# Kernel tuning notes

Measured on AMD Instinct MI355X. Metric: run time of the kernel, lower is better.

The kernel has to match this reference:

```python
import jax, jax.numpy as jnp
import numpy as np
from jax import lax

ALPHA = 0.1
HIDDEN_DIM = 512


def setup_inputs() -> dict:
    key = jax.random.key(0)
    ks = jax.random.split(key, 8)
    B, T, I, H, O, R = 64, 1024, 128, 512, 512, 2
    x = jax.random.normal(ks[0], (B, T, I), dtype=jnp.float32)
    h0 = jnp.zeros((B, H), dtype=jnp.float32)
    Wxh = jax.random.normal(ks[1], (H, I), dtype=jnp.float32) / np.sqrt(I)
    bxh = jax.random.normal(ks[2], (H,), dtype=jnp.float32) * 0.01
    U = jax.random.normal(ks[3], (H, R), dtype=jnp.float32) / np.sqrt(H)
    V = jax.random.normal(ks[4], (H, R), dtype=jnp.float32) / np.sqrt(H)
    Why = jax.random.normal(ks[5], (O, H), dtype=jnp.float32) / np.sqrt(H)
    bhy = jax.random.normal(ks[6], (O,), dtype=jnp.float32) * 0.01
    return {"x": x, "h0": h0, "Wxh": Wxh, "bxh": bxh, "U": U, "V": V,
            "Why": Why, "bhy": bhy}


def reference(x, h0, Wxh, bxh, U, V, Why, bhy):
    # x: (B,T,I); precompute the input projection for all timesteps at once
    xproj = jnp.einsum('bti,hi->bth', x, Wxh) + bxh  # (B,T,H)

    def step(h, xp_t):
        # low-rank recurrent map: h @ V @ U.T / hidden_dim
        pre = xp_t + (h @ V) @ U.T / HIDDEN_DIM  # (B,H)
        h_new = (1.0 - ALPHA) * h + ALPHA * jnp.tanh(pre)
        return h_new, h_new

    _, hs = lax.scan(step, h0, jnp.swapaxes(xproj, 0, 1))  # hs: (T,B,H)
    h_all = jnp.swapaxes(hs, 0, 1)  # (B,T,H)
    y = jnp.einsum('bth,oh->bto', h_all, Why) + bhy  # (B,T,O)
    return y, h_all
```

## Files before the change

### kernel.cpp

```cpp
#include <hip/hip_runtime.h>
#include <hip/hip_bf16.h>
#include <cstdint>

#define B_ 64
#define T_ 1024
#define I_ 128
#define H_ 512
#define O_ 512

#define CHUNK_L 64
#define NCHUNK (T_ / CHUNK_L)
#define WARM_ 96

typedef short bf16x8 __attribute__((ext_vector_type(8)));
typedef float f32x4 __attribute__((ext_vector_type(4)));

typedef const __attribute__((address_space(1))) void* gptr_t;
typedef __attribute__((address_space(3))) void* lptr_t;

__device__ __forceinline__ unsigned short f2bf(float f) {
    unsigned int u = __float_as_uint(f);
    u += 0x7fffu + ((u >> 16) & 1u);
    return (unsigned short)(u >> 16);
}
__device__ __forceinline__ float bf2f(unsigned short b) {
    return __uint_as_float(((unsigned int)b) << 16);
}
__device__ __forceinline__ float fast_tanh(float x) {
    float e = __builtin_amdgcn_exp2f(x * 2.8853900817779268f);
    return 1.0f - 2.0f * __builtin_amdgcn_rcpf(e + 1.0f);
}

template <int CTRL>
__device__ __forceinline__ float dpp_add(float v) {
    int t = __builtin_amdgcn_update_dpp(0, __float_as_int(v), CTRL, 0xf, 0xf, true);
    return v + __int_as_float(t);
}
__device__ __forceinline__ float wave_sum64(float v) {
    v = dpp_add<0x111>(v);
    v = dpp_add<0x112>(v);
    v = dpp_add<0x114>(v);
    v = dpp_add<0x118>(v);
    v = dpp_add<0x142>(v);
    v = dpp_add<0x143>(v);
    return __uint_as_float(__builtin_amdgcn_readlane(__float_as_uint(v), 63));
}

#define NX_ (B_ * T_ * I_)
#define NW_ (H_ * I_)
#define NY_ (O_ * H_)

__global__ __launch_bounds__(256)
void cast_all(const float* __restrict__ x, const float* __restrict__ Wxh,
              const float* __restrict__ Why, unsigned short* __restrict__ xb,
              unsigned short* __restrict__ wb, unsigned short* __restrict__ yb) {
    int i4 = (blockIdx.x * 256 + threadIdx.x) * 4;
    const float* s;
    unsigned short* d;
    int off;
    if (i4 < NX_)             { s = x;   d = xb; off = i4; }
    else if (i4 < NX_ + NW_)  { s = Wxh; d = wb; off = i4 - NX_; }
    else                      { s = Why; d = yb; off = i4 - NX_ - NW_; }
    float4 v = *(const float4*)(s + off);
    ushort4 o;
    o.x = f2bf(v.x); o.y = f2bf(v.y); o.z = f2bf(v.z); o.w = f2bf(v.w);
    *(ushort4*)(d + off) = o;
}

template <bool STORE_BF16>
__global__ __launch_bounds__(256)
void gemm_bt(const unsigned short* __restrict__ A,
             const unsigned short* __restrict__ Bm,
             const float* __restrict__ bias,
             void* __restrict__ Cout,
             int M, int N, int K) {
    __shared__ unsigned short As[128 * 32];
    __shared__ unsigned short Bs[128 * 32];

    const int tid  = threadIdx.x;
    const int lane = tid & 63;
    const int w    = tid >> 6;
    const int wm   = (w >> 1) * 64;
    const int wn   = (w & 1) * 64;
    const int nblk = N >> 7;
    const int bm   = (int)(blockIdx.x / nblk) << 7;
    const int bn   = (int)(blockIdx.x % nblk) << 7;

    f32x4 acc[4][4] = {};

    const int srow = tid >> 2;
    const int scol = (tid & 3) << 3;
    const unsigned short* gA0 = A  + (size_t)(bm + srow) * K + scol;
    const unsigned short* gA1 = A  + (size_t)(bm + 64 + srow) * K + scol;
    const unsigned short* gB0 = Bm + (size_t)(bn + srow) * K + scol;
    const unsigned short* gB1 = Bm + (size_t)(bn + 64 + srow) * K + scol;

    unsigned short* ldsA0 = As + w * 512;
    unsigned short* ldsA1 = As + 2048 + w * 512;
    unsigned short* ldsB0 = Bs + w * 512;
    unsigned short* ldsB1 = Bs + 2048 + w * 512;

    const int frow = lane & 15;
    const int fk   = (lane >> 4) << 3;

    for (int kt = 0; kt < K; kt += 32) {
        __syncthreads();
        __builtin_amdgcn_global_load_lds((gptr_t)(gA0 + kt), (lptr_t)ldsA0, 16, 0, 0);
        __builtin_amdgcn_global_load_lds((gptr_t)(gA1 + kt), (lptr_t)ldsA1, 16, 0, 0);
        __builtin_amdgcn_global_load_lds((gptr_t)(gB0 + kt), (lptr_t)ldsB0, 16, 0, 0);
        __builtin_amdgcn_global_load_lds((gptr_t)(gB1 + kt), (lptr_t)ldsB1, 16, 0, 0);
        __syncthreads();

        bf16x8 af[4], bf[4];
#pragma unroll
        for (int mt = 0; mt < 4; ++mt)
            af[mt] = *(const bf16x8*)(As + (wm + mt * 16 + frow) * 32 + fk);
#pragma unroll
        for (int nt = 0; nt < 4; ++nt)
            bf[nt] = *(const bf16x8*)(Bs + (wn + nt * 16 + frow) * 32 + fk);
#pragma unroll
        for (int mt = 0; mt < 4; ++mt)
#pragma unroll
            for (int nt = 0; nt < 4; ++nt)
                acc[mt][nt] = __builtin_amdgcn_mfma_f32_16x16x32_bf16(
                    af[mt], bf[nt], acc[mt][nt], 0, 0, 0);
    }

    const int c_col = lane & 15;
    const int c_row = (lane >> 4) << 2;
#pragma unroll
    for (int nt = 0; nt < 4; ++nt) {
        const int gn = bn + wn + nt * 16 + c_col;
        const float bv = bias[gn];
#pragma unroll
        for (int mt = 0; mt < 4; ++mt) {
            const int gm0 = bm + wm + mt * 16 + c_row;
#pragma unroll
            for (int r = 0; r < 4; ++r) {
                float v = acc[mt][nt][r] + bv;
                size_t idx = (size_t)(gm0 + r) * N + gn;
                if (STORE_BF16) ((unsigned short*)Cout)[idx] = f2bf(v);
                else            ((float*)Cout)[idx] = v;
            }
        }
    }
}

__global__ __launch_bounds__(64)
void scan_kernel(const unsigned short* __restrict__ xproj,
                 const float* __restrict__ h0,
                 const float* __restrict__ U,
                 const float* __restrict__ V,
                 float* __restrict__ hall_f32,
                 unsigned short* __restrict__ hall_bf) {
    const int blk = blockIdx.x;
    const int b = blk / NCHUNK;
    const int c = blk % NCHUNK;
    const int t_start = c * CHUNK_L;
    const int t0 = (t_start - WARM_ > 0) ? (t_start - WARM_) : 0;
    const int nwarm = t_start - t0;
    const int NT = nwarm + CHUNK_L;

    const int lane = threadIdx.x;
    const int hbase = lane * 8;

    const float inv_h = 1.0f / (float)H_;
    float h[8], V0[8], V1[8], U0[8], U1[8];
#pragma unroll
    for (int j = 0; j < 8; ++j) {
        V0[j] = V[(hbase + j) * 2 + 0] * inv_h;
        V1[j] = V[(hbase + j) * 2 + 1] * inv_h;
        U0[j] = U[(hbase + j) * 2 + 0];
        U1[j] = U[(hbase + j) * 2 + 1];
    }
    if (t0 == 0) {
#pragma unroll
        for (int j = 0; j < 8; ++j) h[j] = h0[b * H_ + hbase + j];
    } else {
#pragma unroll
        for (int j = 0; j < 8; ++j) h[j] = 0.f;
    }

    const unsigned short* xp = xproj + ((size_t)b * T_ + t0) * H_ + hbase;
    float* ho = hall_f32 + (size_t)b * T_ * H_ + hbase;
    unsigned short* hb = hall_bf + (size_t)b * T_ * H_ + hbase;

    float s0 = 0.f, s1 = 0.f;
    if (t0 == 0) {
        float a0 = 0.f, a1 = 0.f;
#pragma unroll
        for (int j = 0; j < 8; ++j) { a0 += h[j] * V0[j]; a1 += h[j] * V1[j]; }
        s0 = wave_sum64(a0);
        s1 = wave_sum64(a1);
    }

    uint4 xq0, xq1, xq2, xq3;
#define LOADX(DST, IDX)                                                        \
    if ((IDX) < NT) DST = *(const uint4*)(xp + (size_t)(IDX) * H_);
    xq0 = *(const uint4*)xp;
    LOADX(xq1, 1)
    LOADX(xq2, 2)
    LOADX(xq3, 3)

#define SCAN_SLOT(REG, IDX, DO_STORE)                                          \
    {                                                                          \
        uint4 xc = REG;                                                        \
        LOADX(REG, (IDX) + 4)                                                  \
        float xp8[8];                                                          \
        {                                                                      \
            unsigned int uu[4] = {xc.x, xc.y, xc.z, xc.w};                     \
            _Pragma("unroll")                                                  \
            for (int q = 0; q < 4; ++q) {                                      \
                xp8[2 * q + 0] = bf2f((unsigned short)(uu[q] & 0xffffu));      \
                xp8[2 * q + 1] = bf2f((unsigned short)(uu[q] >> 16));          \
            }                                                                  \
        }                                                                      \
        float g[8];                                                            \
        _Pragma("unroll")                                                      \
        for (int j = 0; j < 8; ++j)                                            \
            g[j] = fast_tanh(xp8[j] + s0 * U0[j] + s1 * U1[j]);                \
        _Pragma("unroll")                                                      \
        for (int j = 0; j < 8; ++j)                                            \
            h[j] = 0.9f * h[j] + 0.1f * g[j];                                  \
        float p0a = 0.f, p0b = 0.f, p1a = 0.f, p1b = 0.f;                      \
        _Pragma("unroll")                                                      \
        for (int j = 0; j < 4; ++j) {                                          \
            p0a += g[j] * V0[j];       p0b += g[j + 4] * V0[j + 4];            \
            p1a += g[j] * V1[j];       p1b += g[j + 4] * V1[j + 4];            \
        }                                                                      \
        float r0 = wave_sum64(p0a + p0b);                                      \
        float r1 = wave_sum64(p1a + p1b);                                      \
        s0 = 0.9f * s0 + 0.1f * r0;                                            \
        s1 = 0.9f * s1 + 0.1f * r1;                                            \
        if (DO_STORE) {                                                        \
            const size_t tt = (size_t)(t0 + (IDX));                            \
            float4 v0 = make_float4(h[0], h[1], h[2], h[3]);                   \
            float4 v1 = make_float4(h[4], h[5], h[6], h[7]);                   \
            *(float4*)(ho + tt * H_ + 0) = v0;                                 \
            *(float4*)(ho + tt * H_ + 4) = v1;                                 \
            uint4 pb;                                                          \
            pb.x = ((unsigned int)f2bf(h[1]) << 16) | f2bf(h[0]);              \
            pb.y = ((unsigned int)f2bf(h[3]) << 16) | f2bf(h[2]);              \
            pb.z = ((unsigned int)f2bf(h[5]) << 16) | f2bf(h[4]);              \
            pb.w = ((unsigned int)f2bf(h[7]) << 16) | f2bf(h[6]);              \
            *(uint4*)(hb + tt * H_) = pb;                                      \
        }                                                                      \
    }

    int I = 0;
    for (; I < nwarm; I += 4) {
        SCAN_SLOT(xq0, I + 0, false)
        SCAN_SLOT(xq1, I + 1, false)
        SCAN_SLOT(xq2, I + 2, false)
        SCAN_SLOT(xq3, I + 3, false)
    }
    for (; I < NT; I += 4) {
        SCAN_SLOT(xq0, I + 0, true)
        SCAN_SLOT(xq1, I + 1, true)
        SCAN_SLOT(xq2, I + 2, true)
        SCAN_SLOT(xq3, I + 3, true)
    }
#undef SCAN_SLOT
#undef LOADX
}

extern "C" void kernel_launch(void* const* d_in, const int* in_sizes, int n_in,
                              void* d_out, int out_size, void* d_ws, size_t ws_size,
                              hipStream_t stream) {
    const float* x   = (const float*)d_in[0];
    const float* h0  = (const float*)d_in[1];
    const float* Wxh = (const float*)d_in[2];
    const float* bxh = (const float*)d_in[3];
    const float* U   = (const float*)d_in[4];
    const float* V   = (const float*)d_in[5];
    const float* Why = (const float*)d_in[6];
    const float* bhy = (const float*)d_in[7];

    float* y    = (float*)d_out;
    float* hall = y + (size_t)B_ * T_ * O_;

    unsigned short* x_bf    = (unsigned short*)d_ws;
    unsigned short* Wxh_bf  = x_bf + (size_t)B_ * T_ * I_;
    unsigned short* Why_bf  = Wxh_bf + (size_t)H_ * I_;
    unsigned short* xp_bf   = Why_bf + (size_t)O_ * H_;
    unsigned short* hall_bf = xp_bf + (size_t)B_ * T_ * H_;

    cast_all<<<(NX_ + NW_ + NY_) / 1024, 256, 0, stream>>>(
        x, Wxh, Why, x_bf, Wxh_bf, Why_bf);

    gemm_bt<true><<<dim3((B_ * T_ / 128) * (H_ / 128)), 256, 0, stream>>>(
        x_bf, Wxh_bf, bxh, xp_bf, B_ * T_, H_, I_);

    scan_kernel<<<B_ * NCHUNK, 64, 0, stream>>>(xp_bf, h0, U, V, hall, hall_bf);

    gemm_bt<false><<<dim3((B_ * T_ / 128) * (O_ / 128)), 256, 0, stream>>>(
        hall_bf, Why_bf, bhy, y, B_ * T_, O_, H_);
}
```

Measured before the change: 466.7 us.

## Stage GEMM epilogue through padded LDS for coalesced vector stores; branchless scan prefetch

The GEMM epilogue now writes accumulators plus bias into a padded shared-memory tile one 16-row slab at a time, then reads them back so each thread issues 16-byte global stores (float4 or 8 bf16s) instead of scattered scalar stores. This targets the uncoalesced output writes of the input projection and output GEMMs. In exchange it adds LDS usage and two barriers per slab, which may reduce occupancy. Separately, the scan's prefetch loads are made branchless by clamping the index to the last valid timestep, which removes divergent conditionals at the cost of a few redundant loads.

```diff
diff --git a/kernel.cpp b/kernel.cpp
--- a/kernel.cpp
+++ b/kernel.cpp
@@ -67,6 +67,9 @@
     *(ushort4*)(d + off) = o;
 }
 
+#define CPAD_F32 140
+#define CPAD_BF16 136
+
 template <bool STORE_BF16>
 __global__ __launch_bounds__(256)
 void gemm_bt(const unsigned short* __restrict__ A,
@@ -76,6 +79,7 @@
              int M, int N, int K) {
     __shared__ unsigned short As[128 * 32];
     __shared__ unsigned short Bs[128 * 32];
+    __shared__ __align__(16) unsigned char cbuf_raw[32 * CPAD_F32 * 4];
 
     const int tid  = threadIdx.x;
     const int lane = tid & 63;
@@ -128,19 +132,50 @@
 
     const int c_col = lane & 15;
     const int c_row = (lane >> 4) << 2;
-#pragma unroll
-    for (int nt = 0; nt < 4; ++nt) {
-        const int gn = bn + wn + nt * 16 + c_col;
-        const float bv = bias[gn];
-#pragma unroll
-        for (int mt = 0; mt < 4; ++mt) {
-            const int gm0 = bm + wm + mt * 16 + c_row;
-#pragma unroll
-            for (int r = 0; r < 4; ++r) {
-                float v = acc[mt][nt][r] + bv;
-                size_t idx = (size_t)(gm0 + r) * N + gn;
-                if (STORE_BF16) ((unsigned short*)Cout)[idx] = f2bf(v);
-                else            ((float*)Cout)[idx] = v;
+    const int slab  = (w >> 1) << 4;
+    float* cbf = (float*)cbuf_raw;
+    unsigned short* cbh = (unsigned short*)cbuf_raw;
+
+#pragma unroll
+    for (int mt = 0; mt < 4; ++mt) {
+        __syncthreads();
+        if (STORE_BF16) {
+#pragma unroll
+            for (int nt = 0; nt < 4; ++nt) {
+                const int col = wn + nt * 16 + c_col;
+                const float bv = bias[bn + col];
+#pragma unroll
+                for (int r = 0; r < 4; ++r)
+                    cbh[(slab + c_row + r) * CPAD_BF16 + col] = f2bf(acc[mt][nt][r] + bv);
+            }
+        } else {
+#pragma unroll
+            for (int nt = 0; nt < 4; ++nt) {
+                const int col = wn + nt * 16 + c_col;
+                const float bv = bias[bn + col];
+#pragma unroll
+                for (int r = 0; r < 4; ++r)
+                    cbf[(slab + c_row + r) * CPAD_F32 + col] = acc[mt][nt][r] + bv;
+            }
+        }
+        __syncthreads();
+        if (STORE_BF16) {
+#pragma unroll
+            for (int p = 0; p < 2; ++p) {
+                const int lrow = (tid >> 4) + p * 16;
+                const int colg = (tid & 15) * 8;
+                const int grow = bm + (lrow >> 4) * 64 + mt * 16 + (lrow & 15);
+                uint4 vv = *(const uint4*)(cbh + lrow * CPAD_BF16 + colg);
+                *(uint4*)((unsigned short*)Cout + (size_t)grow * N + bn + colg) = vv;
+            }
+        } else {
+#pragma unroll
+            for (int p = 0; p < 4; ++p) {
+                const int lrow = (tid >> 5) + p * 8;
+                const int col4 = (tid & 31) * 4;
+                const int grow = bm + (lrow >> 4) * 64 + mt * 16 + (lrow & 15);
+                float4 vv = *(const float4*)(cbf + lrow * CPAD_F32 + col4);
+                *(float4*)((float*)Cout + (size_t)grow * N + bn + col4) = vv;
             }
         }
     }
@@ -196,8 +231,12 @@
 
     uint4 xq0, xq1, xq2, xq3;
 #define LOADX(DST, IDX)                                                        \
-    if ((IDX) < NT) DST = *(const uint4*)(xp + (size_t)(IDX) * H_);
-    xq0 = *(const uint4*)xp;
+    {                                                                          \
+        int _ii = (IDX);                                                       \
+        _ii = _ii < NT ? _ii : NT - 1;                                         \
+        DST = *(const uint4*)(xp + (size_t)_ii * H_);                          \
+    }
+    LOADX(xq0, 0)
     LOADX(xq1, 1)
     LOADX(xq2, 2)
     LOADX(xq3, 3)
```

After: 452.7 us. -3.0%, faster.
